# Performance work log

Hardware: AMD Instinct MI355X
Metric: run time of the kernel (lower is better)

## Reference

```python
import jax, jax.numpy as jnp
import numpy as np

B, N, D, H = 2, 2048, 768, 12
HD = D // H  # head_dim = 64
SCALE = HD ** -0.5


def setup_inputs() -> dict:
    key = jax.random.key(0)
    ks = jax.random.split(key, 8)
    return {
        "x": jax.random.normal(ks[0], (B, N, D), jnp.float32),
        "masks": jax.random.uniform(ks[1], (B, H, N), jnp.float32),
        "lambda_r": jax.random.uniform(ks[2], (B, H), jnp.float32) * 4.0 + 1.0,
        "theta_r": jax.random.uniform(ks[3], (B, H), jnp.float32),
        "mask_weights": jax.random.uniform(ks[4], (B, H), jnp.float32),
        "qkv_w": jax.random.normal(ks[5], (D, 3 * D), jnp.float32) * (D ** -0.5),
        "qkv_b": jnp.zeros((3 * D,), jnp.float32),
        "proj_w": jax.random.normal(ks[6], (D, D), jnp.float32) * (D ** -0.5),
        "proj_b": jnp.zeros((D,), jnp.float32),
    }


def reference(x, masks, lambda_r, theta_r, mask_weights, qkv_w, qkv_b, proj_w, proj_b):
    # qkv projection: [B,N,3D] -> [3,B,H,N,HD]
    qkv = (x @ qkv_w + qkv_b).reshape(B, N, 3, H, HD).transpose(2, 0, 3, 1, 4)
    q, k, v = qkv[0], qkv[1], qkv[2]
    # raw scores [B,H,N,N]
    attn = jnp.einsum('bhqd,bhkd->bhqk', q, k) * SCALE
    # region gate: sigmoid(lambda * (m_i*m_j - theta)) multiplied into scores pre-softmax
    gate = jax.nn.sigmoid(
        lambda_r[:, :, None, None]
        * (masks[:, :, :, None] * masks[:, :, None, :] - theta_r[:, :, None, None])
    )
    attn = jax.nn.softmax(attn * gate, axis=-1)  # dropout is identity in eval
    out = jnp.einsum('bhqk,bhkd->bqhd', attn, v).reshape(B, N, D)
    # per-head output scaling via mask_weights
    out = out * jnp.repeat(mask_weights, HD, axis=-1)[:, None, :]
    return out @ proj_w + proj_b
```

## Files before the change

### kernel.cpp

```cpp
#include <hip/hip_runtime.h>

typedef unsigned short u16;
typedef unsigned int u32;
typedef __attribute__((ext_vector_type(8))) short short8;
typedef __attribute__((ext_vector_type(4))) float f32x4;

#define NB 2
#define NSEQ 2048
#define DIM 768
#define NH 12
#define HDIM 64

#define LOG2E 1.44269504088896f
#define CFOLD 0.18033688f

#if defined(__has_builtin)
#if __has_builtin(__builtin_amdgcn_exp2f)
#define EXPB(x) __builtin_amdgcn_exp2f(x)
#else
#define EXPB(x) exp2f(x)
#endif
#if __has_builtin(__builtin_amdgcn_rcpf)
#define RCP(x) __builtin_amdgcn_rcpf(x)
#else
#define RCP(x) (1.0f / (x))
#endif
#else
#define EXPB(x) exp2f(x)
#define RCP(x) (1.0f / (x))
#endif

__device__ __forceinline__ u16 f2bf(float x) {
    union { float f; unsigned u; } v; v.f = x;
    unsigned r = v.u + 0x7fffu + ((v.u >> 16) & 1u);
    return (u16)(r >> 16);
}

__device__ __forceinline__ u32 pack_bf16(float a, float b) {
    union { float f; u32 u; } A, B; A.f = a; B.f = b;
    u32 ra = A.u + 0x7fffu + ((A.u >> 16) & 1u);
    u32 rb = B.u + 0x7fffu + ((B.u >> 16) & 1u);
    return __builtin_amdgcn_perm(rb, ra, 0x07060302u);
}

__device__ __forceinline__ f32x4 mfma16(short8 a, short8 b, f32x4 c) {
    return __builtin_amdgcn_mfma_f32_16x16x32_bf16(a, b, c, 0, 0, 0);
}

__device__ __forceinline__ void glds16(const u16* g, u16* l) {
    __builtin_amdgcn_global_load_lds((const __attribute__((address_space(1))) u32*)g,
                                     (__attribute__((address_space(3))) u32*)l, 16, 0, 0);
}

__global__ __launch_bounds__(256) void prep(const float* __restrict__ x, u16* __restrict__ xb,
                                            const float* __restrict__ qkv_w, u16* __restrict__ wq,
                                            const float* __restrict__ proj_w, u16* __restrict__ wp) {
    const int t = threadIdx.x;
    int bid = blockIdx.x;
    if (bid < 3072) {
        int i = (bid * 256 + t) * 4;
        float4 v = *(const float4*)(x + i);
        *(uint2*)(xb + i) = make_uint2(pack_bf16(v.x, v.y), pack_bf16(v.z, v.w));
        return;
    }
    const float* in; u16* outp; int rows, cols, bx, by;
    if (bid < 3072 + 1728) {
        bid -= 3072; in = qkv_w; outp = wq; rows = 768; cols = 2304;
        bx = bid % 72; by = bid / 72;
    } else {
        bid -= 4800; in = proj_w; outp = wp; rows = 768; cols = 768;
        bx = bid % 24; by = bid / 24;
    }
    __shared__ float tile[32][33];
    int c0 = bx * 32, r0 = by * 32;
    int tx = t & 31, ty = t >> 5;
    #pragma unroll
    for (int i = 0; i < 32; i += 8)
        tile[ty + i][tx] = in[(size_t)(r0 + ty + i) * cols + c0 + tx];
    __syncthreads();
    #pragma unroll
    for (int i = 0; i < 32; i += 8)
        outp[(size_t)(c0 + ty + i) * rows + r0 + tx] = f2bf(tile[tx][ty + i]);
}

__global__ __launch_bounds__(256) void vtrans(const u16* __restrict__ vin,
                                              u16* __restrict__ vout) {
    __shared__ __align__(16) u16 tile[64][72];
    const int bh = blockIdx.y;
    const int n0 = blockIdx.x * 64;
    const int t = threadIdx.x;
    const size_t base = (size_t)bh * NSEQ * HDIM;
    int r = t >> 3, cb = (t & 7) * 8;
    *(uint4*)&tile[r][cb]      = *(const uint4*)&vin[base + (size_t)(n0 + r) * HDIM + cb];
    *(uint4*)&tile[r + 32][cb] = *(const uint4*)&vin[base + (size_t)(n0 + r + 32) * HDIM + cb];
    __syncthreads();
    #pragma unroll
    for (int half = 0; half < 2; half++) {
        int d = (t >> 3) + half * 32;
        int nb = (t & 7) * 8;
        short8 v;
        #pragma unroll
        for (int j = 0; j < 8; j++) v[j] = (short)tile[nb + j][d];
        *(short8*)&vout[base + (size_t)d * NSEQ + n0 + nb] = v;
    }
}

__global__ __launch_bounds__(256) void gemm_qkv(const u16* __restrict__ A,
                                                const u16* __restrict__ BT,
                                                const float* __restrict__ bias,
                                                u16* __restrict__ qo,
                                                u16* __restrict__ ko,
                                                u16* __restrict__ vo) {
    __shared__ __align__(16) u16 As[128 * 32];
    __shared__ __align__(16) u16 Bs[128 * 32];
    const int bm = blockIdx.y * 128, bn = blockIdx.x * 128;
    const int t = threadIdx.x;
    const int lane = t & 63, wave = t >> 6;
    const int l15 = lane & 15, quad = lane >> 4;
    const int wm = (wave >> 1) * 64, wn = (wave & 1) * 64;

    const u16* ga = A + (size_t)(bm + (t >> 2)) * DIM + (t & 3) * 8;
    const u16* gb = BT + (size_t)(bn + (t >> 2)) * DIM + (t & 3) * 8;
    u16* la = As + wave * 512;
    u16* lb = Bs + wave * 512;

    f32x4 acc[4][4] = {};
    for (int k0 = 0; k0 < DIM; k0 += 32) {
        __syncthreads();
        glds16(ga, la);
        glds16(ga + (size_t)64 * DIM, la + 2048);
        glds16(gb, lb);
        glds16(gb + (size_t)64 * DIM, lb + 2048);
        ga += 32; gb += 32;
        __syncthreads();
        short8 af[4], bf[4];
        #pragma unroll
        for (int i = 0; i < 4; i++) af[i] = *(const short8*)&As[(wm + i * 16 + l15) * 32 + quad * 8];
        #pragma unroll
        for (int j = 0; j < 4; j++) bf[j] = *(const short8*)&Bs[(wn + j * 16 + l15) * 32 + quad * 8];
        #pragma unroll
        for (int i = 0; i < 4; i++)
            #pragma unroll
            for (int j = 0; j < 4; j++)
                acc[i][j] = mfma16(af[i], bf[j], acc[i][j]);
    }

    #pragma unroll
    for (int i = 0; i < 4; i++) {
        int mr = bm + wm + i * 16 + quad * 4;
        int b = mr >> 11, nn = mr & 2047;
        #pragma unroll
        for (int j = 0; j < 4; j++) {
            int ncol = bn + wn + j * 16 + l15;
            int w = ncol / DIM, rem = ncol - w * DIM;
            int h = rem >> 6, hd = rem & 63;
            u16* dst = (w == 0) ? qo : (w == 1) ? ko : vo;
            float bb = bias[ncol];
            size_t idx = (((size_t)(b * NH + h)) * NSEQ + nn) * HDIM + hd;
            #pragma unroll
            for (int r = 0; r < 4; r++)
                dst[idx + (size_t)r * HDIM] = f2bf(acc[i][j][r] + bb);
        }
    }
}

__global__ __launch_bounds__(128) void attn_kernel(const u16* __restrict__ Q,
                                                   const u16* __restrict__ Kg,
                                                   const u16* __restrict__ Vt,
                                                   const float* __restrict__ masks,
                                                   const float* __restrict__ lambda_r,
                                                   const float* __restrict__ theta_r,
                                                   const float* __restrict__ mask_w,
                                                   u16* __restrict__ AO) {
    const int bh = blockIdx.y;
    const int b = bh / NH, h = bh % NH;
    const int qb = blockIdx.x * 64;
    const int t = threadIdx.x, wave = t >> 6, lane = t & 63;
    const int l15 = lane & 15, quad = lane >> 4;

    __shared__ __align__(16) u16 Ks[64 * 64];
    __shared__ __align__(16) u16 Vs[64 * 64];
    __shared__ __align__(16) u16 Ps[2][2304];
    __shared__ __align__(16) float mks[64];

    const float lam = lambda_r[bh], th = theta_r[bh], mw = mask_w[bh];
    const float Bfac = lam * th * LOG2E;

    const size_t base = (size_t)bh * (NSEQ * HDIM);
    const int qrow = qb + wave * 32;

    short8 bq[2][2];
    float Afac[2], lsum[2];
    #pragma unroll
    for (int g = 0; g < 2; g++) {
        const u16* Qr = Q + base + (size_t)(qrow + g * 16 + l15) * HDIM;
        bq[g][0] = *(const short8*)(Qr + quad * 8);
        bq[g][1] = *(const short8*)(Qr + 32 + quad * 8);
        float mq = masks[bh * NSEQ + qrow + g * 16 + l15];
        Afac[g] = -lam * LOG2E * mq;
        lsum[g] = 0.f;
    }
    f32x4 O[2][4] = {};

    const int srow = t >> 3, scb = t & 7;
    const int gcb = scb ^ (srow & 7);
    const u16* kgp = Kg + base + (size_t)srow * HDIM + gcb * 8;
    const u16* vgp = Vt + base + (size_t)srow * NSEQ + gcb * 8;
    u16* ksl = Ks + wave * 512;
    u16* vsl = Vs + wave * 512;

    const int ph = (quad ^ (l15 & 7)) * 8;
    const int kb0 = l15 * 64 + ph, kb1 = l15 * 64 + (ph ^ 32);
    u16* PsW = Ps[wave];
    const int pw = l15 * 72 + quad * 4;
    const int prd = l15 * 72 + quad * 8;

    const float* mrow = masks + bh * NSEQ;

    for (int kt = 0; kt < NSEQ / 64; kt++) {
        __syncthreads();
        #pragma unroll
        for (int i = 0; i < 4; i++) glds16(kgp + i * 16 * HDIM, ksl + i * 1024);
        #pragma unroll
        for (int i = 0; i < 4; i++) glds16(vgp + (size_t)i * 16 * NSEQ, vsl + i * 1024);
        if (t < 16) *(float4*)&mks[t * 4] = *(const float4*)&mrow[kt * 64 + t * 4];
        kgp += 64 * HDIM; vgp += 64;
        __syncthreads();

        #pragma unroll
        for (int c = 0; c < 4; c++) {
            short8 ak0 = *(const short8*)&Ks[kb0 + c * 1024];
            short8 ak1 = *(const short8*)&Ks[kb1 + c * 1024];
            float4 mkv = *(const float4*)&mks[c * 16 + quad * 4];
            #pragma unroll
            for (int g = 0; g < 2; g++) {
                f32x4 S = {0.f, 0.f, 0.f, 0.f};
                S = mfma16(ak0, bq[g][0], S);
                S = mfma16(ak1, bq[g][1], S);
                float p[4];
                #pragma unroll
                for (int r = 0; r < 4; r++) {
                    float mk = (r == 0) ? mkv.x : (r == 1) ? mkv.y : (r == 2) ? mkv.z : mkv.w;
                    float e = EXPB(fmaf(mk, Afac[g], Bfac));
                    float gate = RCP(1.0f + e);
                    p[r] = EXPB(S[r] * CFOLD * gate);
                }
                lsum[g] += (p[0] + p[1]) + (p[2] + p[3]);
                *(uint2*)&PsW[g * 1152 + pw + c * 16] =
                    make_uint2(pack_bf16(p[0], p[1]), pack_bf16(p[2], p[3]));
            }
        }

        #pragma unroll
        for (int kc = 0; kc < 2; kc++) {
            const int vb = kc ? kb1 : kb0;
            short8 bp0 = *(const short8*)&PsW[prd + kc * 32];
            short8 bp1 = *(const short8*)&PsW[1152 + prd + kc * 32];
            #pragma unroll
            for (int dt = 0; dt < 4; dt++) {
                short8 av = *(const short8*)&Vs[vb + dt * 1024];
                O[0][dt] = mfma16(av, bp0, O[0][dt]);
                O[1][dt] = mfma16(av, bp1, O[1][dt]);
            }
        }
    }

    #pragma unroll
    for (int g = 0; g < 2; g++) {
        float ls = lsum[g];
        ls += __shfl_xor(ls, 16);
        ls += __shfl_xor(ls, 32);
        float sc = mw / ls;
        u16* aor = AO + ((size_t)(b * NSEQ) + qrow + g * 16 + l15) * DIM + h * HDIM + quad * 4;
        #pragma unroll
        for (int dt = 0; dt < 4; dt++) {
            *(uint2*)(aor + dt * 16) = make_uint2(pack_bf16(O[g][dt][0] * sc, O[g][dt][1] * sc),
                                                  pack_bf16(O[g][dt][2] * sc, O[g][dt][3] * sc));
        }
    }
}

__global__ __launch_bounds__(256) void gemm_proj(const u16* __restrict__ A,
                                                 const u16* __restrict__ BT,
                                                 const float* __restrict__ bias,
                                                 float* __restrict__ outp) {
    __shared__ __align__(16) u16 As[128 * 32];
    __shared__ __align__(16) u16 Bs[64 * 32];
    const int bm = blockIdx.y * 128, bn = blockIdx.x * 64;
    const int t = threadIdx.x;
    const int lane = t & 63, wave = t >> 6;
    const int l15 = lane & 15, quad = lane >> 4;
    const int wm = wave * 32;

    const u16* ga = A + (size_t)(bm + (t >> 2)) * DIM + (t & 3) * 8;
    const u16* gb = BT + (size_t)(bn + (t >> 2)) * DIM + (t & 3) * 8;
    u16* la = As + wave * 512;
    u16* lb = Bs + wave * 512;

    f32x4 acc[2][4] = {};
    for (int k0 = 0; k0 < DIM; k0 += 32) {
        __syncthreads();
        glds16(ga, la);
        glds16(ga + (size_t)64 * DIM, la + 2048);
        glds16(gb, lb);
        ga += 32; gb += 32;
        __syncthreads();
        short8 af[2], bf[4];
        #pragma unroll
        for (int i = 0; i < 2; i++) af[i] = *(const short8*)&As[(wm + i * 16 + l15) * 32 + quad * 8];
        #pragma unroll
        for (int j = 0; j < 4; j++) bf[j] = *(const short8*)&Bs[(j * 16 + l15) * 32 + quad * 8];
        #pragma unroll
        for (int i = 0; i < 2; i++)
            #pragma unroll
            for (int j = 0; j < 4; j++)
                acc[i][j] = mfma16(af[i], bf[j], acc[i][j]);
    }

    #pragma unroll
    for (int i = 0; i < 2; i++) {
        int mr = bm + wm + i * 16 + quad * 4;
        #pragma unroll
        for (int j = 0; j < 4; j++) {
            int ncol = bn + j * 16 + l15;
            float bb = bias[ncol];
            #pragma unroll
            for (int r = 0; r < 4; r++)
                outp[(size_t)(mr + r) * DIM + ncol] = acc[i][j][r] + bb;
        }
    }
}

extern "C" void kernel_launch(void* const* d_in, const int* in_sizes, int n_in,
                              void* d_out, int out_size, void* d_ws, size_t ws_size,
                              hipStream_t stream) {
    const float* x            = (const float*)d_in[0];
    const float* masks        = (const float*)d_in[1];
    const float* lambda_r     = (const float*)d_in[2];
    const float* theta_r      = (const float*)d_in[3];
    const float* mask_weights = (const float*)d_in[4];
    const float* qkv_w        = (const float*)d_in[5];
    const float* qkv_b        = (const float*)d_in[6];
    const float* proj_w       = (const float*)d_in[7];
    const float* proj_b       = (const float*)d_in[8];
    float* outp = (float*)d_out;

    const size_t SZH = (size_t)NB * NH * NSEQ * HDIM;
    u16* xb    = (u16*)d_ws;
    u16* wqkvT = xb + (size_t)4096 * 768;
    u16* wprT  = wqkvT + (size_t)2304 * 768;
    u16* qg    = wprT + (size_t)768 * 768;
    u16* kg    = qg + SZH;
    u16* vtmp  = kg + SZH;
    u16* vt    = vtmp + SZH;
    u16* ao    = xb;

    prep<<<dim3(3072 + 1728 + 576), 256, 0, stream>>>(x, xb, qkv_w, wqkvT, proj_w, wprT);
    gemm_qkv<<<dim3(2304 / 128, 4096 / 128), 256, 0, stream>>>(xb, wqkvT, qkv_b, qg, kg, vtmp);
    vtrans<<<dim3(NSEQ / 64, NB * NH), 256, 0, stream>>>(vtmp, vt);
    attn_kernel<<<dim3(NSEQ / 64, NB * NH), 128, 0, stream>>>(qg, kg, vt, masks, lambda_r,
                                                              theta_r, mask_weights, ao);
    gemm_proj<<<dim3(768 / 64, 4096 / 128), 256, 0, stream>>>(ao, wprT, proj_b, outp);
}
```

Measured before the change: 218.9 us.

## Double-buffer LDS tiles in GEMMs and attention; swizzle GEMM LDS; 4-wave attention

Both GEMMs and the attention kernel now use double-buffered LDS, so the next K/V or A/B tile is loaded while the current one is computed, with one barrier per iteration instead of two. The GEMM LDS layout is XOR-swizzled to reduce bank conflicts on the fragment reads. The attention block grows to 256 threads with each wave handling 16 query rows instead of 32, which halves per-wave register state and spreads the tile loads over more threads. This doubles LDS use per block and lowers per-wave reuse of each loaded K/V tile.

```diff
diff --git a/kernel.cpp b/kernel.cpp
--- a/kernel.cpp
+++ b/kernel.cpp
@@ -111,33 +111,40 @@
                                                 u16* __restrict__ qo,
                                                 u16* __restrict__ ko,
                                                 u16* __restrict__ vo) {
-    __shared__ __align__(16) u16 As[128 * 32];
-    __shared__ __align__(16) u16 Bs[128 * 32];
+    __shared__ __align__(16) u16 As[2][4096];
+    __shared__ __align__(16) u16 Bs[2][4096];
     const int bm = blockIdx.y * 128, bn = blockIdx.x * 128;
     const int t = threadIdx.x;
     const int lane = t & 63, wave = t >> 6;
     const int l15 = lane & 15, quad = lane >> 4;
     const int wm = (wave >> 1) * 64, wn = (wave & 1) * 64;
 
-    const u16* ga = A + (size_t)(bm + (t >> 2)) * DIM + (t & 3) * 8;
-    const u16* gb = BT + (size_t)(bn + (t >> 2)) * DIM + (t & 3) * 8;
-    u16* la = As + wave * 512;
-    u16* lb = Bs + wave * 512;
+    const int srow = t >> 2;
+    const int sc = (t & 3) ^ ((srow >> 1) & 3);
+    const u16* ga = A + (size_t)(bm + srow) * DIM + sc * 8;
+    const u16* gb = BT + (size_t)(bn + srow) * DIM + sc * 8;
+    const int ldst = wave * 512;
+    const int swz = (quad ^ ((l15 >> 1) & 3)) * 8;
 
     f32x4 acc[4][4] = {};
-    for (int k0 = 0; k0 < DIM; k0 += 32) {
+    glds16(ga, &As[0][ldst]); glds16(ga + (size_t)64 * DIM, &As[0][2048 + ldst]);
+    glds16(gb, &Bs[0][ldst]); glds16(gb + (size_t)64 * DIM, &Bs[0][2048 + ldst]);
+    ga += 32; gb += 32;
+
+    const int NKT = DIM / 32;
+    for (int kt = 0; kt < NKT; kt++) {
+        const int buf = kt & 1;
         __syncthreads();
-        glds16(ga, la);
-        glds16(ga + (size_t)64 * DIM, la + 2048);
-        glds16(gb, lb);
-        glds16(gb + (size_t)64 * DIM, lb + 2048);
-        ga += 32; gb += 32;
-        __syncthreads();
+        if (kt + 1 < NKT) {
+            glds16(ga, &As[buf ^ 1][ldst]); glds16(ga + (size_t)64 * DIM, &As[buf ^ 1][2048 + ldst]);
+            glds16(gb, &Bs[buf ^ 1][ldst]); glds16(gb + (size_t)64 * DIM, &Bs[buf ^ 1][2048 + ldst]);
+            ga += 32; gb += 32;
+        }
         short8 af[4], bf[4];
         #pragma unroll
-        for (int i = 0; i < 4; i++) af[i] = *(const short8*)&As[(wm + i * 16 + l15) * 32 + quad * 8];
-        #pragma unroll
-        for (int j = 0; j < 4; j++) bf[j] = *(const short8*)&Bs[(wn + j * 16 + l15) * 32 + quad * 8];
+        for (int i = 0; i < 4; i++) af[i] = *(const short8*)&As[buf][(wm + i * 16 + l15) * 32 + swz];
+        #pragma unroll
+        for (int j = 0; j < 4; j++) bf[j] = *(const short8*)&Bs[buf][(wn + j * 16 + l15) * 32 + swz];
         #pragma unroll
         for (int i = 0; i < 4; i++)
             #pragma unroll
@@ -164,7 +171,7 @@
     }
 }
 
-__global__ __launch_bounds__(128) void attn_kernel(const u16* __restrict__ Q,
+__global__ __launch_bounds__(256) void attn_kernel(const u16* __restrict__ Q,
                                                    const u16* __restrict__ Kg,
                                                    const u16* __restrict__ Vt,
                                                    const float* __restrict__ masks,
@@ -178,105 +185,101 @@
     const int t = threadIdx.x, wave = t >> 6, lane = t & 63;
     const int l15 = lane & 15, quad = lane >> 4;
 
-    __shared__ __align__(16) u16 Ks[64 * 64];
-    __shared__ __align__(16) u16 Vs[64 * 64];
-    __shared__ __align__(16) u16 Ps[2][2304];
-    __shared__ __align__(16) float mks[64];
+    __shared__ __align__(16) u16 Ks[2][4096];
+    __shared__ __align__(16) u16 Vs[2][4096];
+    __shared__ __align__(16) u16 Ps[4][1152];
+    __shared__ __align__(16) float mks[2][64];
 
     const float lam = lambda_r[bh], th = theta_r[bh], mw = mask_w[bh];
     const float Bfac = lam * th * LOG2E;
 
     const size_t base = (size_t)bh * (NSEQ * HDIM);
-    const int qrow = qb + wave * 32;
-
-    short8 bq[2][2];
-    float Afac[2], lsum[2];
-    #pragma unroll
-    for (int g = 0; g < 2; g++) {
-        const u16* Qr = Q + base + (size_t)(qrow + g * 16 + l15) * HDIM;
-        bq[g][0] = *(const short8*)(Qr + quad * 8);
-        bq[g][1] = *(const short8*)(Qr + 32 + quad * 8);
-        float mq = masks[bh * NSEQ + qrow + g * 16 + l15];
-        Afac[g] = -lam * LOG2E * mq;
-        lsum[g] = 0.f;
-    }
-    f32x4 O[2][4] = {};
-
-    const int srow = t >> 3, scb = t & 7;
-    const int gcb = scb ^ (srow & 7);
-    const u16* kgp = Kg + base + (size_t)srow * HDIM + gcb * 8;
-    const u16* vgp = Vt + base + (size_t)srow * NSEQ + gcb * 8;
-    u16* ksl = Ks + wave * 512;
-    u16* vsl = Vs + wave * 512;
+    const int qrow = qb + wave * 16;
+
+    const u16* Qr = Q + base + (size_t)(qrow + l15) * HDIM;
+    short8 bq0 = *(const short8*)(Qr + quad * 8);
+    short8 bq1 = *(const short8*)(Qr + 32 + quad * 8);
+    const float Afac = -lam * LOG2E * masks[bh * NSEQ + qrow + l15];
+
+    const int srow = t >> 3;
+    const int gc = (t & 7) ^ (srow & 7);
+    const u16* kgp = Kg + base + (size_t)srow * HDIM + gc * 8;
+    const u16* vgp = Vt + base + (size_t)srow * NSEQ + gc * 8;
+    const int ldst = wave * 512;
 
     const int ph = (quad ^ (l15 & 7)) * 8;
     const int kb0 = l15 * 64 + ph, kb1 = l15 * 64 + (ph ^ 32);
     u16* PsW = Ps[wave];
     const int pw = l15 * 72 + quad * 4;
     const int prd = l15 * 72 + quad * 8;
-
     const float* mrow = masks + bh * NSEQ;
 
-    for (int kt = 0; kt < NSEQ / 64; kt++) {
+    float lsum = 0.f;
+    f32x4 O[4] = {};
+
+    glds16(kgp, &Ks[0][ldst]);
+    glds16(kgp + 32 * HDIM, &Ks[0][2048 + ldst]);
+    glds16(vgp, &Vs[0][ldst]);
+    glds16(vgp + (size_t)32 * NSEQ, &Vs[0][2048 + ldst]);
+    if (t < 16) *(float4*)&mks[0][t * 4] = *(const float4*)&mrow[t * 4];
+
+    const int NT = NSEQ / 64;
+    for (int kt = 0; kt < NT; kt++) {
+        const int buf = kt & 1;
         __syncthreads();
-        #pragma unroll
-        for (int i = 0; i < 4; i++) glds16(kgp + i * 16 * HDIM, ksl + i * 1024);
-        #pragma unroll
-        for (int i = 0; i < 4; i++) glds16(vgp + (size_t)i * 16 * NSEQ, vsl + i * 1024);
-        if (t < 16) *(float4*)&mks[t * 4] = *(const float4*)&mrow[kt * 64 + t * 4];
-        kgp += 64 * HDIM; vgp += 64;
-        __syncthreads();
+        if (kt + 1 < NT) {
+            const u16* kn = kgp + (kt + 1) * 64 * HDIM;
+            const u16* vn = vgp + (kt + 1) * 64;
+            glds16(kn, &Ks[buf ^ 1][ldst]);
+            glds16(kn + 32 * HDIM, &Ks[buf ^ 1][2048 + ldst]);
+            glds16(vn, &Vs[buf ^ 1][ldst]);
+            glds16(vn + (size_t)32 * NSEQ, &Vs[buf ^ 1][2048 + ldst]);
+            if (t < 16) *(float4*)&mks[buf ^ 1][t * 4] = *(const float4*)&mrow[(kt + 1) * 64 + t * 4];
+        }
+        const u16* KsB = Ks[buf];
+        const u16* VsB = Vs[buf];
+        const float* mkb = mks[buf];
 
         #pragma unroll
         for (int c = 0; c < 4; c++) {
-            short8 ak0 = *(const short8*)&Ks[kb0 + c * 1024];
-            short8 ak1 = *(const short8*)&Ks[kb1 + c * 1024];
-            float4 mkv = *(const float4*)&mks[c * 16 + quad * 4];
-            #pragma unroll
-            for (int g = 0; g < 2; g++) {
-                f32x4 S = {0.f, 0.f, 0.f, 0.f};
-                S = mfma16(ak0, bq[g][0], S);
-                S = mfma16(ak1, bq[g][1], S);
-                float p[4];
-                #pragma unroll
-                for (int r = 0; r < 4; r++) {
-                    float mk = (r == 0) ? mkv.x : (r == 1) ? mkv.y : (r == 2) ? mkv.z : mkv.w;
-                    float e = EXPB(fmaf(mk, Afac[g], Bfac));
-                    float gate = RCP(1.0f + e);
-                    p[r] = EXPB(S[r] * CFOLD * gate);
-                }
-                lsum[g] += (p[0] + p[1]) + (p[2] + p[3]);
-                *(uint2*)&PsW[g * 1152 + pw + c * 16] =
-                    make_uint2(pack_bf16(p[0], p[1]), pack_bf16(p[2], p[3]));
+            short8 ak0 = *(const short8*)&KsB[kb0 + c * 1024];
+            short8 ak1 = *(const short8*)&KsB[kb1 + c * 1024];
+            f32x4 S = {0.f, 0.f, 0.f, 0.f};
+            S = mfma16(ak0, bq0, S);
+            S = mfma16(ak1, bq1, S);
+            float4 mkv = *(const float4*)&mkb[c * 16 + quad * 4];
+            float p[4];
+            #pragma unroll
+            for (int r = 0; r < 4; r++) {
+                float mk = (r == 0) ? mkv.x : (r == 1) ? mkv.y : (r == 2) ? mkv.z : mkv.w;
+                float e = EXPB(fmaf(mk, Afac, Bfac));
+                float gate = RCP(1.0f + e);
+                p[r] = EXPB(S[r] * CFOLD * gate);
             }
+            lsum += (p[0] + p[1]) + (p[2] + p[3]);
+            *(uint2*)&PsW[pw + c * 16] = make_uint2(pack_bf16(p[0], p[1]), pack_bf16(p[2], p[3]));
         }
 
         #pragma unroll
         for (int kc = 0; kc < 2; kc++) {
             const int vb = kc ? kb1 : kb0;
-            short8 bp0 = *(const short8*)&PsW[prd + kc * 32];
-            short8 bp1 = *(const short8*)&PsW[1152 + prd + kc * 32];
+            short8 bp = *(const short8*)&PsW[prd + kc * 32];
             #pragma unroll
             for (int dt = 0; dt < 4; dt++) {
-                short8 av = *(const short8*)&Vs[vb + dt * 1024];
-                O[0][dt] = mfma16(av, bp0, O[0][dt]);
-                O[1][dt] = mfma16(av, bp1, O[1][dt]);
+                short8 av = *(const short8*)&VsB[vb + dt * 1024];
+                O[dt] = mfma16(av, bp, O[dt]);
             }
         }
     }
 
-    #pragma unroll
-    for (int g = 0; g < 2; g++) {
-        float ls = lsum[g];
-        ls += __shfl_xor(ls, 16);
-        ls += __shfl_xor(ls, 32);
-        float sc = mw / ls;
-        u16* aor = AO + ((size_t)(b * NSEQ) + qrow + g * 16 + l15) * DIM + h * HDIM + quad * 4;
-        #pragma unroll
-        for (int dt = 0; dt < 4; dt++) {
-            *(uint2*)(aor + dt * 16) = make_uint2(pack_bf16(O[g][dt][0] * sc, O[g][dt][1] * sc),
-                                                  pack_bf16(O[g][dt][2] * sc, O[g][dt][3] * sc));
-        }
+    lsum += __shfl_xor(lsum, 16);
+    lsum += __shfl_xor(lsum, 32);
+    float sc = mw / lsum;
+    u16* aor = AO + ((size_t)(b * NSEQ) + qrow + l15) * DIM + h * HDIM + quad * 4;
+    #pragma unroll
+    for (int dt = 0; dt < 4; dt++) {
+        *(uint2*)(aor + dt * 16) = make_uint2(pack_bf16(O[dt][0] * sc, O[dt][1] * sc),
+                                              pack_bf16(O[dt][2] * sc, O[dt][3] * sc));
     }
 }
 
@@ -284,32 +287,40 @@
                                                  const u16* __restrict__ BT,
                                                  const float* __restrict__ bias,
                                                  float* __restrict__ outp) {
-    __shared__ __align__(16) u16 As[128 * 32];
-    __shared__ __align__(16) u16 Bs[64 * 32];
+    __shared__ __align__(16) u16 As[2][4096];
+    __shared__ __align__(16) u16 Bs[2][2048];
     const int bm = blockIdx.y * 128, bn = blockIdx.x * 64;
     const int t = threadIdx.x;
     const int lane = t & 63, wave = t >> 6;
     const int l15 = lane & 15, quad = lane >> 4;
     const int wm = wave * 32;
 
-    const u16* ga = A + (size_t)(bm + (t >> 2)) * DIM + (t & 3) * 8;
-    const u16* gb = BT + (size_t)(bn + (t >> 2)) * DIM + (t & 3) * 8;
-    u16* la = As + wave * 512;
-    u16* lb = Bs + wave * 512;
+    const int srow = t >> 2;
+    const int sc = (t & 3) ^ ((srow >> 1) & 3);
+    const u16* ga = A + (size_t)(bm + srow) * DIM + sc * 8;
+    const u16* gb = BT + (size_t)(bn + srow) * DIM + sc * 8;
+    const int ldst = wave * 512;
+    const int swz = (quad ^ ((l15 >> 1) & 3)) * 8;
 
     f32x4 acc[2][4] = {};
-    for (int k0 = 0; k0 < DIM; k0 += 32) {
+    glds16(ga, &As[0][ldst]); glds16(ga + (size_t)64 * DIM, &As[0][2048 + ldst]);
+    glds16(gb, &Bs[0][ldst]);
+    ga += 32; gb += 32;
+
+    const int NKT = DIM / 32;
+    for (int kt = 0; kt < NKT; kt++) {
+        const int buf = kt & 1;
         __syncthreads();
-        glds16(ga, la);
-        glds16(ga + (size_t)64 * DIM, la + 2048);
-        glds16(gb, lb);
-        ga += 32; gb += 32;
-        __syncthreads();
+        if (kt + 1 < NKT) {
+            glds16(ga, &As[buf ^ 1][ldst]); glds16(ga + (size_t)64 * DIM, &As[buf ^ 1][2048 + ldst]);
+            glds16(gb, &Bs[buf ^ 1][ldst]);
+            ga += 32; gb += 32;
+        }
         short8 af[2], bf[4];
         #pragma unroll
-        for (int i = 0; i < 2; i++) af[i] = *(const short8*)&As[(wm + i * 16 + l15) * 32 + quad * 8];
-        #pragma unroll
-        for (int j = 0; j < 4; j++) bf[j] = *(const short8*)&Bs[(j * 16 + l15) * 32 + quad * 8];
+        for (int i = 0; i < 2; i++) af[i] = *(const short8*)&As[buf][(wm + i * 16 + l15) * 32 + swz];
+        #pragma unroll
+        for (int j = 0; j < 4; j++) bf[j] = *(const short8*)&Bs[buf][(j * 16 + l15) * 32 + swz];
         #pragma unroll
         for (int i = 0; i < 2; i++)
             #pragma unroll
@@ -358,7 +369,7 @@
     prep<<<dim3(3072 + 1728 + 576), 256, 0, stream>>>(x, xb, qkv_w, wqkvT, proj_w, wprT);
     gemm_qkv<<<dim3(2304 / 128, 4096 / 128), 256, 0, stream>>>(xb, wqkvT, qkv_b, qg, kg, vtmp);
     vtrans<<<dim3(NSEQ / 64, NB * NH), 256, 0, stream>>>(vtmp, vt);
-    attn_kernel<<<dim3(NSEQ / 64, NB * NH), 128, 0, stream>>>(qg, kg, vt, masks, lambda_r,
+    attn_kernel<<<dim3(NSEQ / 64, NB * NH), 256, 0, stream>>>(qg, kg, vt, masks, lambda_r,
                                                               theta_r, mask_weights, ao);
     gemm_proj<<<dim3(768 / 64, 4096 / 128), 256, 0, stream>>>(ao, wprT, proj_b, outp);
 }
```

Measured after the change: 202.2 us. -7.6%, faster.
